# Performance work log

Measured on AMD Instinct MI355X. Metric: run time of the kernel, lower is better.

Reference implementation:

```python
import jax, jax.numpy as jnp
import numpy as np

EMBED_DIM = 2048
NUM_HEADS = 16
HEAD_DIM = EMBED_DIM // NUM_HEADS  # 128


def setup_inputs() -> dict:
    key = jax.random.key(0)
    ks = jax.random.split(key, 11)
    B, S, D, Hd = 2, 2048, EMBED_DIM, HEAD_DIM
    s_in = 1.0 / np.sqrt(D)
    return {
        "query": jax.random.normal(ks[0], (B, S, D), dtype=jnp.float32),
        "key": jax.random.normal(ks[1], (B, S, D), dtype=jnp.float32),
        "value": jax.random.normal(ks[2], (B, S, D), dtype=jnp.float32),
        "Wq": jax.random.normal(ks[3], (D, D), dtype=jnp.float32) * s_in,
        "bq": jax.random.normal(ks[4], (D,), dtype=jnp.float32) * s_in,
        "Wk": jax.random.normal(ks[5], (D, Hd), dtype=jnp.float32) * s_in,
        "bk": jax.random.normal(ks[6], (Hd,), dtype=jnp.float32) * s_in,
        "Wv": jax.random.normal(ks[7], (D, Hd), dtype=jnp.float32) * s_in,
        "bv": jax.random.normal(ks[8], (Hd,), dtype=jnp.float32) * s_in,
        "Wo": jax.random.normal(ks[9], (D, D), dtype=jnp.float32) * s_in,
        "bo": jax.random.normal(ks[10], (D,), dtype=jnp.float32) * s_in,
    }


def reference(query, key, value, Wq, bq, Wk, bk, Wv, bv, Wo, bo):
    B, S, D = query.shape
    H, Hd = NUM_HEADS, HEAD_DIM
    # projections
    Q = (query @ Wq + bq).reshape(B, S, H, Hd).transpose(0, 2, 1, 3)  # [B,H,S,Hd]
    K = key @ Wk + bk    # [B,S,Hd] single shared KV head
    V = value @ Wv + bv  # [B,S,Hd]
    scale = 1.0 / jnp.sqrt(jnp.asarray(Hd, dtype=Q.dtype))
    # MQA: broadcast single K/V head across H query heads
    scores = jnp.einsum("bhsd,btd->bhst", Q, K) * scale  # [B,H,S,S]
    attn = jax.nn.softmax(scores, axis=-1)
    out = jnp.einsum("bhst,btd->bhsd", attn, V)  # [B,H,S,Hd]
    out = out.transpose(0, 2, 1, 3).reshape(B, S, D)
    return out @ Wo + bo
```

## Files before the change

kernel.cpp:

```cpp
#include <hip/hip_runtime.h>
#include <stdint.h>

#define S_LEN 2048
#define EMBED 2048
#define NHEADS 16
#define HDIM 128

typedef __attribute__((ext_vector_type(8))) short bf16x8;
typedef __attribute__((ext_vector_type(4))) float f32x4;
typedef unsigned short us;

static __device__ __forceinline__ us f2b(float f) {
    union { float f; unsigned u; } x; x.f = f;
    unsigned r = x.u + 0x7fffu + ((x.u >> 16) & 1u);
    return (us)(r >> 16);
}

static __device__ __forceinline__ unsigned cvtpk(float a, float b) {
    unsigned r;
    asm("v_cvt_pk_bf16_f32 %0, %1, %2" : "=v"(r) : "v"(a), "v"(b));
    return r;
}

static __device__ __forceinline__ uint2 pack4(float a, float b, float c, float d) {
    uint2 u;
    u.x = cvtpk(a, b);
    u.y = cvtpk(c, d);
    return u;
}

static __device__ __forceinline__ float fexp2(float x) {
    float r;
    asm("v_exp_f32 %0, %1" : "=v"(r) : "v"(x));
    return r;
}

static __device__ __forceinline__ void gl_lds16(const void* g, void* l) {
    __builtin_amdgcn_global_load_lds(
        (const __attribute__((address_space(1))) void*)g,
        (__attribute__((address_space(3))) void*)l, 16, 0, 0);
}


static __device__ __forceinline__ void dma_tile(const us* __restrict__ g, int k0,
                                                us* dst, int tid) {
#pragma unroll
    for (int i = 0; i < 4; i++) {
        int sl = i * 256 + tid;
        int row = sl >> 3, cp = sl & 7, c = cp ^ (row & 7);
        gl_lds16(g + (size_t)row * 2048 + k0 + c * 8,
                 (char*)dst + (i * 256 + (tid & 192)) * 16);
    }
}

static __device__ __forceinline__ void loadA_f32(const float* __restrict__ g,
                                                 float4 pf[8]) {
#pragma unroll
    for (int i = 0; i < 8; i++) pf[i] = ((const float4*)g)[i];
}

static __device__ __forceinline__ void writeA_f32(us* dst, const float4 pf[8],
                                                  int row, int h) {
#pragma unroll
    for (int cc = 0; cc < 4; cc++) {
        int p = (h * 4 + cc) ^ (row & 7);
        float4 a = pf[cc * 2], b = pf[cc * 2 + 1];
        uint4 u;
        u.x = (unsigned)f2b(a.x) | ((unsigned)f2b(a.y) << 16);
        u.y = (unsigned)f2b(a.z) | ((unsigned)f2b(a.w) << 16);
        u.z = (unsigned)f2b(b.x) | ((unsigned)f2b(b.y) << 16);
        u.w = (unsigned)f2b(b.z) | ((unsigned)f2b(b.w) << 16);
        *(uint4*)&dst[row * 64 + p * 8] = u;
    }
}

static __device__ __forceinline__ void frag_mfma(const us* curA, const us* curB,
                                                 int wm, int wn, int lm, int quad,
                                                 f32x4 acc[4][4]) {
#pragma unroll
    for (int kc = 0; kc < 2; kc++) {
        bf16x8 af[4], bfr[4];
#pragma unroll
        for (int mi = 0; mi < 4; mi++) {
            int row = wm * 64 + mi * 16 + lm;
            int p = (kc * 4 + quad) ^ (row & 7);
            af[mi] = *(const bf16x8*)&curA[row * 64 + p * 8];
        }
#pragma unroll
        for (int ni = 0; ni < 4; ni++) {
            int row = wn * 64 + ni * 16 + lm;
            int p = (kc * 4 + quad) ^ (row & 7);
            bfr[ni] = *(const bf16x8*)&curB[row * 64 + p * 8];
        }
#pragma unroll
        for (int mi = 0; mi < 4; mi++)
#pragma unroll
            for (int ni = 0; ni < 4; ni++)
                acc[mi][ni] = __builtin_amdgcn_mfma_f32_16x16x32_bf16(
                    af[mi], bfr[ni], acc[mi][ni], 0, 0, 0);
    }
}

__global__ void tcast3(const float* __restrict__ Wq, const float* __restrict__ Wk,
                       const float* __restrict__ Wv, const float* __restrict__ query,
                       us* __restrict__ Wqt, us* __restrict__ Wkvt,
                       us* __restrict__ qbf) {
    int b = blockIdx.x;
    if (b >= 2304) {
        int id = (b - 2304) * 256 + threadIdx.x;
        const float4* in4 = (const float4*)query;
        float4 a = in4[id * 2], c = in4[id * 2 + 1];
        uint4 u;
        u.x = (unsigned)f2b(a.x) | ((unsigned)f2b(a.y) << 16);
        u.y = (unsigned)f2b(a.z) | ((unsigned)f2b(a.w) << 16);
        u.z = (unsigned)f2b(c.x) | ((unsigned)f2b(c.y) << 16);
        u.w = (unsigned)f2b(c.z) | ((unsigned)f2b(c.w) << 16);
        ((uint4*)qbf)[id] = u;
        return;
    }
    const float* in; us* out; int N, rel;
    if (b < 2048)      { in = Wq; out = Wqt;  N = 2048; rel = b; }
    else if (b < 2176) { in = Wk; out = Wkvt; N = 128;  rel = b - 2048; }
    else               { in = Wv; out = Wkvt + (size_t)128 * 2048; N = 128; rel = b - 2176; }
    int id = rel * 256 + threadIdx.x;
    int n = id & (N - 1), k0 = (id / N) * 8;
    us t8[8];
#pragma unroll
    for (int j = 0; j < 8; j++) t8[j] = f2b(in[(size_t)(k0 + j) * N + n]);
    *(uint4*)&out[(size_t)n * 2048 + k0] = *(uint4*)t8;
}

__global__ __launch_bounds__(256, 2) void proj_qkv(
    const float* __restrict__ key, const float* __restrict__ value,
    const us* __restrict__ qbf, const us* __restrict__ Wqt,
    const us* __restrict__ Wkvt, const float* __restrict__ bq,
    us* __restrict__ Qh, float* __restrict__ part)
{
    __shared__ __align__(16) us A0[128 * 64], A1[128 * 64];
    __shared__ __align__(16) us B0[128 * 64], B1[128 * 64];

    const int tid = threadIdx.x;
    const int lane = tid & 63, w = tid >> 6, lm = lane & 15, quad = lane >> 4;
    const int wm = w >> 1, wn = w & 1;
    const int id = blockIdx.x;
    const float CQ = 0.12751743150179665f;

    f32x4 acc[4][4];
#pragma unroll
    for (int i = 0; i < 4; i++)
#pragma unroll
        for (int j = 0; j < 4; j++) acc[i][j] = (f32x4){0.f, 0.f, 0.f, 0.f};

    if (id < 512) {
        const int bn = (id & 15) * 128, bm = (id >> 4) * 128;
        const us* Atile = qbf + (size_t)bm * 2048;
        const us* Btile = Wqt + (size_t)bn * 2048;

        dma_tile(Atile, 0, A0, tid);
        dma_tile(Btile, 0, B0, tid);

        for (int kk = 0; kk < 32; kk += 2) {
            __syncthreads();
            if (kk + 1 < 32) { dma_tile(Atile, (kk + 1) * 64, A1, tid);
                               dma_tile(Btile, (kk + 1) * 64, B1, tid); }
            frag_mfma(A0, B0, wm, wn, lm, quad, acc);
            __syncthreads();
            if (kk + 2 < 32) { dma_tile(Atile, (kk + 2) * 64, A0, tid);
                               dma_tile(Btile, (kk + 2) * 64, B0, tid); }
            frag_mfma(A1, B1, wm, wn, lm, quad, acc);
        }

#pragma unroll
        for (int mi = 0; mi < 4; mi++)
#pragma unroll
            for (int ni = 0; ni < 4; ni++) {
                int col = bn + wn * 64 + ni * 16 + lm;
                float bv = bq[col];
#pragma unroll
                for (int r = 0; r < 4; r++) {
                    int row = bm + wm * 64 + mi * 16 + quad * 4 + r;
                    float v = (acc[mi][ni][r] + bv) * CQ;
                    int b = row >> 11, s = row & 2047;
                    int hh = col >> 7, hd = col & 127;
                    size_t addr = (((size_t)(b * 16 + hh) * 2048 + s) << 7)
                                  + (((hd >> 3) ^ (s & 7)) << 3) + (hd & 7);
                    Qh[addr] = f2b(v);
                }
            }
    } else {
        int e = id - 512;
        int z = e >> 6, r = e & 63, isV = r & 1;
        int bm = (r >> 1) * 128, bn = isV * 128;
        const float* Atile = (isV ? value : key) + (size_t)bm * 2048;
        const us* Btile = Wkvt + (size_t)bn * 2048;
        const int kbeg = z * 512, iters = 8;
        const int arow = tid >> 1, h = tid & 1;
        const float* Ag = Atile + (size_t)arow * 2048 + h * 32;

        float4 pf[8];
        loadA_f32(Ag + kbeg, pf);
        dma_tile(Btile, kbeg, B0, tid);
        writeA_f32(A0, pf, arow, h);

        for (int kk = 0; kk < iters; kk += 2) {
            const int k1 = kbeg + (kk + 1) * 64;
            const int k2 = kbeg + (kk + 2) * 64;
            __syncthreads();
            if (kk + 1 < iters) { loadA_f32(Ag + k1, pf); dma_tile(Btile, k1, B1, tid); }
            frag_mfma(A0, B0, wm, wn, lm, quad, acc);
            if (kk + 1 < iters) writeA_f32(A1, pf, arow, h);
            __syncthreads();
            if (kk + 2 < iters) { loadA_f32(Ag + k2, pf); dma_tile(Btile, k2, B0, tid); }
            frag_mfma(A1, B1, wm, wn, lm, quad, acc);
            if (kk + 2 < iters) writeA_f32(A0, pf, arow, h);
        }

        float* pp = part + (size_t)z * 1048576;
#pragma unroll
        for (int mi = 0; mi < 4; mi++)
#pragma unroll
            for (int ni = 0; ni < 4; ni++) {
                int col = bn + wn * 64 + ni * 16 + lm;
#pragma unroll
                for (int r = 0; r < 4; r++) {
                    int row = bm + wm * 64 + mi * 16 + quad * 4 + r;
                    pp[(size_t)row * 256 + col] = acc[mi][ni][r];
                }
            }
    }
}

__global__ void finish_wot(const float* __restrict__ part, const float* __restrict__ bk,
                           const float* __restrict__ bv, us* __restrict__ Kb,
                           us* __restrict__ Vt, const float* __restrict__ Wo,
                           us* __restrict__ Wot) {
    int b = blockIdx.x;
    if (b < 2048) {
        int id = b * 256 + threadIdx.x;
        int n = id & 2047, k0 = (id >> 11) * 8;
        us t8[8];
#pragma unroll
        for (int j = 0; j < 8; j++) t8[j] = f2b(Wo[(size_t)(k0 + j) * 2048 + n]);
        *(uint4*)&Wot[(size_t)n * 2048 + k0] = *(uint4*)t8;
    } else {
        int id = (b - 2048) * 256 + threadIdx.x;
        int row = id >> 8, n = id & 255;
        float s = part[id] + part[1048576 + id] + part[2097152 + id] + part[3145728 + id];
        int bb = row >> 11, t = row & 2047;
        if (n < 128) {
            int hd = n;
            s += bk[hd];
            Kb[((size_t)(bb * 2048 + t) << 7) + (((hd >> 3) ^ (t & 7)) << 3) + (hd & 7)] = f2b(s);
        } else {
            int hd = n - 128;
            s += bv[hd];
            size_t addr = (((size_t)(bb * 64 + (t >> 5)) * 128 + hd) << 5)
                          + ((((t >> 3) & 3) ^ ((hd >> 1) & 3)) << 3) + (t & 7);
            Vt[addr] = f2b(s);
        }
    }
}

__global__ __launch_bounds__(256, 2) void mqa_attn(
    const us* __restrict__ Qh, const us* __restrict__ Kb,
    const us* __restrict__ Vt, us* __restrict__ AO)
{
    __shared__ __align__(16) char smem[33792];
    us* Ps  = (us*)smem;
    us* Vts = (us*)(smem + 16384);
    float* Lb = (float*)(smem + 32768);

    const int tid  = threadIdx.x;
    const int lane = tid & 63;
    const int w    = tid >> 6;
    const int lm   = lane & 15;
    const int quad = lane >> 4;
    const int wm = w >> 1, wn = w & 1;
    const int q0 = blockIdx.x * 128;
    const int h  = blockIdx.y;
    const int b  = blockIdx.z;

    const us* Qtile = Qh + (((size_t)(b * 16 + h) * 2048 + q0) << 7);
    const us* Kbase = Kb + ((size_t)b * 2048 << 7);
    const us* Vbase = Vt + (size_t)b * 64 * 4096;

#pragma unroll
    for (int i = 0; i < 2; i++) {
        int sl = w * 128 + i * 64 + lane;
        gl_lds16(Vbase + sl * 8, (char*)Vts + (w * 128 + i * 64) * 16);
    }

    bf16x8 qf[4][4];
#pragma unroll
    for (int nt = 0; nt < 4; nt++)
#pragma unroll
        for (int ks = 0; ks < 4; ks++) {
            int q = wn * 64 + nt * 16 + lm;
            int cp = (ks * 4 + quad) ^ (q & 7);
            qf[nt][ks] = *(const bf16x8*)&Qtile[q * 128 + cp * 8];
        }

    const int trow = wm * 16 + lm;
    bf16x8 kfc[4], kfn[4];
#pragma unroll
    for (int ks = 0; ks < 4; ks++) {
        int cp = (ks * 4 + quad) ^ (lm & 7);
        kfc[ks] = *(const bf16x8*)&Kbase[(size_t)trow * 128 + cp * 8];
    }

    __syncthreads();

    f32x4 oacc[4][4];
#pragma unroll
    for (int i = 0; i < 4; i++)
#pragma unroll
        for (int j = 0; j < 4; j++) oacc[i][j] = (f32x4){0.f, 0.f, 0.f, 0.f};
    float lsum[4] = {0.f, 0.f, 0.f, 0.f};

    for (int it = 0; it < 64; ++it) {
        const int p = it & 1;

        if (it < 63) {
            const us* kg = Kbase + (size_t)(it + 1) * 4096 + (size_t)trow * 128;
#pragma unroll
            for (int ks = 0; ks < 4; ks++) {
                int cp = (ks * 4 + quad) ^ (lm & 7);
                kfn[ks] = *(const bf16x8*)&kg[cp * 8];
            }
        }

        f32x4 sacc[4];
#pragma unroll
        for (int nt = 0; nt < 4; nt++) sacc[nt] = (f32x4){0.f, 0.f, 0.f, 0.f};
        __builtin_amdgcn_s_setprio(1);
#pragma unroll
        for (int ks = 0; ks < 4; ks++) {
#pragma unroll
            for (int nt = 0; nt < 4; nt++)
                sacc[nt] = __builtin_amdgcn_mfma_f32_16x16x32_bf16(
                    kfc[ks], qf[nt][ks], sacc[nt], 0, 0, 0);
        }
        __builtin_amdgcn_s_setprio(0);

        us* Pw = Ps + p * 4096;
#pragma unroll
        for (int nt = 0; nt < 4; nt++) {
            int q = wn * 64 + nt * 16 + lm;
            float p0 = fexp2(sacc[nt][0]);
            float p1 = fexp2(sacc[nt][1]);
            float p2 = fexp2(sacc[nt][2]);
            float p3 = fexp2(sacc[nt][3]);
            lsum[nt] += (p0 + p1) + (p2 + p3);
            int tb = wm * 16 + quad * 4;
            int cp = (tb >> 3) ^ ((q >> 1) & 3);
            *(uint2*)&Pw[q * 32 + cp * 8 + (tb & 7)] = pack4(p0, p1, p2, p3);
        }

        __syncthreads();

        if (it < 63) {
            const us* vg = Vbase + (it + 1) * 4096;
#pragma unroll
            for (int i = 0; i < 2; i++) {
                int sl = w * 128 + i * 64 + lane;
                gl_lds16(vg + sl * 8, (char*)Vts + (1 - p) * 8192 + (w * 128 + i * 64) * 16);
            }
        }

        const us* Vst = Vts + p * 4096;
        const us* Pr = Ps + p * 4096;
        bf16x8 vf[4], pfr[4];
#pragma unroll
        for (int mt = 0; mt < 4; mt++) {
            int hd = (wm * 4 + mt) * 16 + lm;
            int cp = quad ^ ((hd >> 1) & 3);
            vf[mt] = *(const bf16x8*)&Vst[hd * 32 + cp * 8];
        }
#pragma unroll
        for (int nt = 0; nt < 4; nt++) {
            int q = (wn * 4 + nt) * 16 + lm;
            int cp = quad ^ ((q >> 1) & 3);
            pfr[nt] = *(const bf16x8*)&Pr[q * 32 + cp * 8];
        }
        __builtin_amdgcn_s_setprio(1);
#pragma unroll
        for (int mt = 0; mt < 4; mt++)
#pragma unroll
            for (int nt = 0; nt < 4; nt++)
                oacc[mt][nt] = __builtin_amdgcn_mfma_f32_16x16x32_bf16(
                    vf[mt], pfr[nt], oacc[mt][nt], 0, 0, 0);
        __builtin_amdgcn_s_setprio(0);

#pragma unroll
        for (int ks = 0; ks < 4; ks++) kfc[ks] = kfn[ks];
    }

#pragma unroll
    for (int nt = 0; nt < 4; nt++) {
        lsum[nt] += __shfl_xor(lsum[nt], 16);
        lsum[nt] += __shfl_xor(lsum[nt], 32);
    }
    if (quad == 0) {
#pragma unroll
        for (int nt = 0; nt < 4; nt++)
            Lb[wm * 128 + wn * 64 + nt * 16 + lm] = lsum[nt];
    }
    __syncthreads();

#pragma unroll
    for (int nt = 0; nt < 4; nt++) {
        int q = (wn * 4 + nt) * 16 + lm;
        float linv = 1.f / (Lb[q] + Lb[128 + q]);
#pragma unroll
        for (int mt = 0; mt < 4; mt++) {
            int hdb = (wm * 4 + mt) * 16 + quad * 4;
            uint2 u = pack4(oacc[mt][nt][0] * linv, oacc[mt][nt][1] * linv,
                            oacc[mt][nt][2] * linv, oacc[mt][nt][3] * linv);
            *(uint2*)&AO[((size_t)(b * 2048 + q0 + q)) * 2048 + h * 128 + hdb] = u;
        }
    }
}

__global__ __launch_bounds__(256, 2) void oproj(
    const us* __restrict__ AO, const us* __restrict__ Wot,
    const float* __restrict__ bo, float* __restrict__ out)
{
    __shared__ __align__(16) us A0[128 * 64], A1[128 * 64];
    __shared__ __align__(16) us B0[128 * 64], B1[128 * 64];

    const int tid = threadIdx.x;
    const int lane = tid & 63, w = tid >> 6, lm = lane & 15, quad = lane >> 4;
    const int wm = w >> 1, wn = w & 1;
    const int bn = blockIdx.x * 128, bm = blockIdx.y * 128;
    const us* Atile = AO + (size_t)bm * 2048;
    const us* Btile = Wot + (size_t)bn * 2048;

    f32x4 acc[4][4];
#pragma unroll
    for (int i = 0; i < 4; i++)
#pragma unroll
        for (int j = 0; j < 4; j++) acc[i][j] = (f32x4){0.f, 0.f, 0.f, 0.f};

    dma_tile(Atile, 0, A0, tid);
    dma_tile(Btile, 0, B0, tid);

    for (int kk = 0; kk < 32; kk += 2) {
        __syncthreads();
        if (kk + 1 < 32) { dma_tile(Atile, (kk + 1) * 64, A1, tid);
                           dma_tile(Btile, (kk + 1) * 64, B1, tid); }
        frag_mfma(A0, B0, wm, wn, lm, quad, acc);
        __syncthreads();
        if (kk + 2 < 32) { dma_tile(Atile, (kk + 2) * 64, A0, tid);
                           dma_tile(Btile, (kk + 2) * 64, B0, tid); }
        frag_mfma(A1, B1, wm, wn, lm, quad, acc);
    }

#pragma unroll
    for (int mi = 0; mi < 4; mi++)
#pragma unroll
        for (int ni = 0; ni < 4; ni++) {
            int col = bn + wn * 64 + ni * 16 + lm;
            float bv = bo[col];
#pragma unroll
            for (int r = 0; r < 4; r++) {
                int row = bm + wm * 64 + mi * 16 + quad * 4 + r;
                out[(size_t)row * 2048 + col] = acc[mi][ni][r] + bv;
            }
        }
}

extern "C" void kernel_launch(void* const* d_in, const int* in_sizes, int n_in,
                              void* d_out, int out_size, void* d_ws, size_t ws_size,
                              hipStream_t stream) {
    const float* query = (const float*)d_in[0];
    const float* key   = (const float*)d_in[1];
    const float* value = (const float*)d_in[2];
    const float* Wq = (const float*)d_in[3];
    const float* bq = (const float*)d_in[4];
    const float* Wk = (const float*)d_in[5];
    const float* bk = (const float*)d_in[6];
    const float* Wv = (const float*)d_in[7];
    const float* bv = (const float*)d_in[8];
    const float* Wo = (const float*)d_in[9];
    const float* bo = (const float*)d_in[10];
    float* out = (float*)d_out;

    char* ws = (char*)d_ws;
    us*    Wqt  = (us*)ws;
    us*    Wot  = Wqt;
    us*    Wkvt = (us*)(ws + 8388608);
    us*    Qh   = (us*)(ws + 9437184);
    float* part = (float*)(ws + 26214400);
    us*    AO   = (us*)part;
    us*    Kb   = (us*)(ws + 42991616);
    us*    Vtb  = (us*)(ws + 44040192);
    us*    qbf  = (us*)(ws + 45088768);

    dim3 blk(256);
    tcast3<<<6400, blk, 0, stream>>>(Wq, Wk, Wv, query, Wqt, Wkvt, qbf);
    proj_qkv<<<768, blk, 0, stream>>>(key, value, qbf, Wqt, Wkvt, bq, Qh, part);
    finish_wot<<<6144, blk, 0, stream>>>(part, bk, bv, Kb, Vtb, Wo, Wot);
    mqa_attn<<<dim3(16, 16, 2), blk, 0, stream>>>(Qh, Kb, Vtb, AO);
    oproj<<<dim3(16, 32), blk, 0, stream>>>(AO, Wot, bo, out);
}
```

Before: 333.4 us.

## Single-buffer projection GEMMs for higher occupancy and unroll attention K double-buffer

The Q/KV projection and output projection GEMMs drop LDS double buffering in favour of a single shared tile with load, sync and compute stages, and raise launch bounds from 2 to 4 blocks per CU. The aim is to rely on more resident waves, rather than intra-block prefetch, to hide memory latency. The attention loop is manually unrolled by two with ping-pong K fragment registers, which removes the per-iteration register copy. The risk is exposed load latency per block and tighter register limits under the higher occupancy target, which could cause spills.

```diff
diff --git a/kernel.cpp b/kernel.cpp
--- a/kernel.cpp
+++ b/kernel.cpp
@@ -130,14 +130,14 @@
     *(uint4*)&out[(size_t)n * 2048 + k0] = *(uint4*)t8;
 }
 
-__global__ __launch_bounds__(256, 2) void proj_qkv(
+__global__ __launch_bounds__(256, 4) void proj_qkv(
     const float* __restrict__ key, const float* __restrict__ value,
     const us* __restrict__ qbf, const us* __restrict__ Wqt,
     const us* __restrict__ Wkvt, const float* __restrict__ bq,
     us* __restrict__ Qh, float* __restrict__ part)
 {
-    __shared__ __align__(16) us A0[128 * 64], A1[128 * 64];
-    __shared__ __align__(16) us B0[128 * 64], B1[128 * 64];
+    __shared__ __align__(16) us A0[128 * 64];
+    __shared__ __align__(16) us B0[128 * 64];
 
     const int tid = threadIdx.x;
     const int lane = tid & 63, w = tid >> 6, lm = lane & 15, quad = lane >> 4;
@@ -156,18 +156,12 @@
         const us* Atile = qbf + (size_t)bm * 2048;
         const us* Btile = Wqt + (size_t)bn * 2048;
 
-        dma_tile(Atile, 0, A0, tid);
-        dma_tile(Btile, 0, B0, tid);
-
-        for (int kk = 0; kk < 32; kk += 2) {
+        for (int kk = 0; kk < 32; kk++) {
             __syncthreads();
-            if (kk + 1 < 32) { dma_tile(Atile, (kk + 1) * 64, A1, tid);
-                               dma_tile(Btile, (kk + 1) * 64, B1, tid); }
+            dma_tile(Atile, kk * 64, A0, tid);
+            dma_tile(Btile, kk * 64, B0, tid);
+            __syncthreads();
             frag_mfma(A0, B0, wm, wn, lm, quad, acc);
-            __syncthreads();
-            if (kk + 2 < 32) { dma_tile(Atile, (kk + 2) * 64, A0, tid);
-                               dma_tile(Btile, (kk + 2) * 64, B0, tid); }
-            frag_mfma(A1, B1, wm, wn, lm, quad, acc);
         }
 
 #pragma unroll
@@ -193,26 +187,18 @@
         int bm = (r >> 1) * 128, bn = isV * 128;
         const float* Atile = (isV ? value : key) + (size_t)bm * 2048;
         const us* Btile = Wkvt + (size_t)bn * 2048;
-        const int kbeg = z * 512, iters = 8;
+        const int kbeg = z * 512;
         const int arow = tid >> 1, h = tid & 1;
         const float* Ag = Atile + (size_t)arow * 2048 + h * 32;
 
-        float4 pf[8];
-        loadA_f32(Ag + kbeg, pf);
-        dma_tile(Btile, kbeg, B0, tid);
-        writeA_f32(A0, pf, arow, h);
-
-        for (int kk = 0; kk < iters; kk += 2) {
-            const int k1 = kbeg + (kk + 1) * 64;
-            const int k2 = kbeg + (kk + 2) * 64;
+        for (int kk = 0; kk < 8; kk++) {
+            float4 pf[8];
+            loadA_f32(Ag + kbeg + kk * 64, pf);
             __syncthreads();
-            if (kk + 1 < iters) { loadA_f32(Ag + k1, pf); dma_tile(Btile, k1, B1, tid); }
+            writeA_f32(A0, pf, arow, h);
+            dma_tile(Btile, kbeg + kk * 64, B0, tid);
+            __syncthreads();
             frag_mfma(A0, B0, wm, wn, lm, quad, acc);
-            if (kk + 1 < iters) writeA_f32(A1, pf, arow, h);
-            __syncthreads();
-            if (kk + 2 < iters) { loadA_f32(Ag + k2, pf); dma_tile(Btile, k2, B0, tid); }
-            frag_mfma(A1, B1, wm, wn, lm, quad, acc);
-            if (kk + 2 < iters) writeA_f32(A0, pf, arow, h);
         }
 
         float* pp = part + (size_t)z * 1048576;
@@ -301,11 +287,11 @@
         }
 
     const int trow = wm * 16 + lm;
-    bf16x8 kfc[4], kfn[4];
+    bf16x8 kfA[4], kfB[4];
 #pragma unroll
     for (int ks = 0; ks < 4; ks++) {
         int cp = (ks * 4 + quad) ^ (lm & 7);
-        kfc[ks] = *(const bf16x8*)&Kbase[(size_t)trow * 128 + cp * 8];
+        kfA[ks] = *(const bf16x8*)&Kbase[(size_t)trow * 128 + cp * 8];
     }
 
     __syncthreads();
@@ -317,9 +303,7 @@
         for (int j = 0; j < 4; j++) oacc[i][j] = (f32x4){0.f, 0.f, 0.f, 0.f};
     float lsum[4] = {0.f, 0.f, 0.f, 0.f};
 
-    for (int it = 0; it < 64; ++it) {
-        const int p = it & 1;
-
+    auto attn_iter = [&](int it, int p, bf16x8 (&kfc)[4], bf16x8 (&kfn)[4]) {
         if (it < 63) {
             const us* kg = Kbase + (size_t)(it + 1) * 4096 + (size_t)trow * 128;
 #pragma unroll
@@ -390,9 +374,11 @@
                 oacc[mt][nt] = __builtin_amdgcn_mfma_f32_16x16x32_bf16(
                     vf[mt], pfr[nt], oacc[mt][nt], 0, 0, 0);
         __builtin_amdgcn_s_setprio(0);
-
-#pragma unroll
-        for (int ks = 0; ks < 4; ks++) kfc[ks] = kfn[ks];
+    };
+
+    for (int it = 0; it < 64; it += 2) {
+        attn_iter(it, 0, kfA, kfB);
+        attn_iter(it + 1, 1, kfB, kfA);
     }
 
 #pragma unroll
@@ -421,12 +407,12 @@
     }
 }
 
-__global__ __launch_bounds__(256, 2) void oproj(
+__global__ __launch_bounds__(256, 4) void oproj(
     const us* __restrict__ AO, const us* __restrict__ Wot,
     const float* __restrict__ bo, float* __restrict__ out)
 {
-    __shared__ __align__(16) us A0[128 * 64], A1[128 * 64];
-    __shared__ __align__(16) us B0[128 * 64], B1[128 * 64];
+    __shared__ __align__(16) us A0[128 * 64];
+    __shared__ __align__(16) us B0[128 * 64];
 
     const int tid = threadIdx.x;
     const int lane = tid & 63, w = tid >> 6, lm = lane & 15, quad = lane >> 4;
@@ -441,18 +427,12 @@
 #pragma unroll
         for (int j = 0; j < 4; j++) acc[i][j] = (f32x4){0.f, 0.f, 0.f, 0.f};
 
-    dma_tile(Atile, 0, A0, tid);
-    dma_tile(Btile, 0, B0, tid);
-
-    for (int kk = 0; kk < 32; kk += 2) {
+    for (int kk = 0; kk < 32; kk++) {
         __syncthreads();
-        if (kk + 1 < 32) { dma_tile(Atile, (kk + 1) * 64, A1, tid);
-                           dma_tile(Btile, (kk + 1) * 64, B1, tid); }
+        dma_tile(Atile, kk * 64, A0, tid);
+        dma_tile(Btile, kk * 64, B0, tid);
+        __syncthreads();
         frag_mfma(A0, B0, wm, wn, lm, quad, acc);
-        __syncthreads();
-        if (kk + 2 < 32) { dma_tile(Atile, (kk + 2) * 64, A0, tid);
-                           dma_tile(Btile, (kk + 2) * 64, B0, tid); }
-        frag_mfma(A1, B1, wm, wn, lm, quad, acc);
     }
 
 #pragma unroll
```

New measurement: 336.1 us. Within noise of the previous version (+0.8%).
